# Optimization experiments

Measured on AMD Instinct MI355X. Metric: run time of the kernel, lower is better.

Reference implementation:

```python
import jax, jax.numpy as jnp
import numpy as np

RADIUS_IN = 0.05
RADIUS_OUT = 0.2
NSAMPLE = 32


def setup_inputs() -> dict:
    key = jax.random.key(0)
    k1, k2, k3 = jax.random.split(key, 3)
    B, N, M, C = 2, 16384, 2048, 64
    xyz = jax.random.uniform(k1, (B, N, 3), dtype=jnp.float32)
    new_xyz = jax.random.uniform(k2, (B, M, 3), dtype=jnp.float32)
    features = jax.random.normal(k3, (B, C, N), dtype=jnp.float32)
    return {"xyz": xyz, "new_xyz": new_xyz, "features": features}


def _ball_query_dilated(xyz, new_xyz, r_in, r_out, nsample):
    # xyz: (B,N,3), new_xyz: (B,M,3)
    d2 = jnp.sum((new_xyz[:, :, None, :] - xyz[:, None, :, :]) ** 2, axis=-1)  # (B,M,N)
    mask = (d2 >= r_in * r_in) & (d2 < r_out * r_out)  # dilated shell
    B, M, N = mask.shape
    rank = jnp.cumsum(mask, axis=-1) - 1  # order of each match along N
    cnt = jnp.minimum(jnp.sum(mask, axis=-1), nsample).astype(jnp.int32)  # (B,M)
    # scatter the j-th point index into slot `rank` (overflow slots dumped into pad)
    pos = jnp.where(mask & (rank < nsample), rank, nsample)
    b = jnp.arange(B)[:, None, None]
    m = jnp.arange(M)[None, :, None]
    j = jnp.broadcast_to(jnp.arange(N, dtype=jnp.int32)[None, None, :], (B, M, N))
    idx = jnp.zeros((B, M, nsample + 1), jnp.int32).at[b, m, pos].set(j)[..., :nsample]
    # CUDA kernel fills unused slots with the FIRST matched index (0 if no match)
    slot = jnp.arange(nsample)[None, None, :]
    idx = jnp.where(slot < cnt[..., None], idx, idx[..., :1])
    return cnt, idx


def _group(features, idx):
    # features: (B,C,N), idx: (B,M,S) -> (B,C,M,S)
    B, C, N = features.shape
    _, M, S = idx.shape
    flat = idx.reshape(B, 1, M * S)
    return jnp.take_along_axis(features, flat, axis=2).reshape(B, C, M, S)


def reference(xyz, new_xyz, features):
    idx_cnt, idx = _ball_query_dilated(xyz, new_xyz, RADIUS_IN, RADIUS_OUT, NSAMPLE)
    xyz_t = jnp.transpose(xyz, (0, 2, 1))            # (B,3,N)
    grouped_xyz = _group(xyz_t, idx)                 # (B,3,M,S)
    grouped_xyz = grouped_xyz - jnp.transpose(new_xyz, (0, 2, 1))[..., None]
    grouped_features = _group(features, idx)         # (B,C,M,S)
    new_features = jnp.concatenate([grouped_xyz, grouped_features], axis=1)
    return idx_cnt, new_features
```

## Files before the change

### kernel.cpp

```cpp
#include <hip/hip_runtime.h>
#include <cstdint>

#define BB 2
#define NN 16384
#define MM 2048
#define CC 64
#define SS 32
#define WPB 4

__device__ __forceinline__ float dist2(float qx, float qy, float qz,
                                       float px, float py, float pz) {
    float dx = __fsub_rn(qx, px), dy = __fsub_rn(qy, py), dz = __fsub_rn(qz, pz);
    return __fadd_rn(__fadd_rn(__fmul_rn(dx, dx), __fmul_rn(dy, dy)), __fmul_rn(dz, dz));
}

__global__ __launch_bounds__(256) void prep_fused(
    const float* __restrict__ xyz, const float* __restrict__ f,
    float* __restrict__ ft, float4* __restrict__ xyz4) {
    int bid = blockIdx.x;
    if (bid < 2048) {
        __shared__ float tile[32][33];
        int n0 = (bid & 511) * 32;
        int c0 = ((bid >> 9) & 1) * 32;
        int b = bid >> 10;
        int tx = threadIdx.x & 31, ty = threadIdx.x >> 5;
#pragma unroll
        for (int k = 0; k < 32; k += 8)
            tile[ty + k][tx] = f[((size_t)(b * CC + c0 + ty + k)) * NN + n0 + tx];
        __syncthreads();
#pragma unroll
        for (int k = 0; k < 32; k += 8)
            ft[((size_t)(b * NN + n0 + ty + k)) * CC + c0 + tx] = tile[tx][ty + k];
    } else {
        int i = (bid - 2048) * 256 + threadIdx.x;
        if (i < BB * NN) {
            xyz4[i] = make_float4(xyz[3 * i], xyz[3 * i + 1], xyz[3 * i + 2], 0.f);
        }
    }
}

template <bool FAST>
__global__ __launch_bounds__(64 * WPB) void query_group(
    const float* __restrict__ xyz, const float* __restrict__ new_xyz,
    const float* __restrict__ features, const float* __restrict__ feat_t,
    const float4* __restrict__ xyz4, float* __restrict__ out) {
    constexpr float R_IN2 = 0.05f * 0.05f;
    constexpr float R_OUT2 = 0.2f * 0.2f;
    __shared__ int idxS[WPB][SS];
    __shared__ float fbuf[WPB][SS][CC + 4];

    int lane = threadIdx.x & 63;
    int w = threadIdx.x >> 6;
    int bm = blockIdx.x * WPB + w;
    int b = bm >> 11;
    int m = bm & 2047;

    float qx = new_xyz[(size_t)bm * 3 + 0];
    float qy = new_xyz[(size_t)bm * 3 + 1];
    float qz = new_xyz[(size_t)bm * 3 + 2];

    if (lane == 0) idxS[w][0] = 0;

    unsigned long long below = (1ull << lane) - 1ull;
    int cnt = 0;
    for (int j0 = 0; j0 < NN; j0 += 256) {
        float px[4], py[4], pz[4];
        if (FAST) {
            const float4* base = xyz4 + b * NN + j0 + lane;
#pragma unroll
            for (int u = 0; u < 4; ++u) {
                float4 p = base[u * 64];
                px[u] = p.x; py[u] = p.y; pz[u] = p.z;
            }
        } else {
            const float* pp = xyz + ((size_t)(b * NN + j0 + lane)) * 3;
#pragma unroll
            for (int u = 0; u < 4; ++u) {
                px[u] = pp[u * 192 + 0];
                py[u] = pp[u * 192 + 1];
                pz[u] = pp[u * 192 + 2];
            }
        }
#pragma unroll
        for (int u = 0; u < 4; ++u) {
            float d2 = dist2(qx, qy, qz, px[u], py[u], pz[u]);
            bool inshell = (d2 >= R_IN2) && (d2 < R_OUT2);
            unsigned long long mk = __ballot(inshell);
            if (inshell) {
                int r = cnt + __popcll(mk & below);
                if (r < SS) idxS[w][r] = j0 + u * 64 + lane;
            }
            cnt += __popcll(mk);
        }
        if (cnt >= SS) break;
    }
    if (cnt > SS) cnt = SS;
    if (lane == 0) out[bm] = (float)cnt;

    float* gout = out + BB * MM;

    if (FAST) {
        int s4 = lane >> 4, c4 = lane & 15;
#pragma unroll
        for (int it = 0; it < 8; ++it) {
            int sl = it * 4 + s4;
            int j = (sl < cnt) ? idxS[w][sl] : idxS[w][0];
            const float4* src = (const float4*)(feat_t + ((size_t)b * NN + j) * CC);
            float4 v = src[c4];
            *((float4*)&fbuf[w][sl][c4 * 4]) = v;
        }
    }

    int s = lane & 31, half = lane >> 5;
    int j = (s < cnt) ? idxS[w][s] : idxS[w][0];

    float px, py, pz;
    if (FAST) {
        float4 p = xyz4[b * NN + j];
        px = p.x; py = p.y; pz = p.z;
    } else {
        const float* pp = xyz + ((size_t)(b * NN) + j) * 3;
        px = pp[0]; py = pp[1]; pz = pp[2];
    }

    {
        float v01 = half ? __fsub_rn(py, qy) : __fsub_rn(px, qx);
        gout[((size_t)(b * 67 + half) * MM + m) * SS + s] = v01;
        if (half == 0) {
            gout[((size_t)(b * 67 + 2) * MM + m) * SS + s] = __fsub_rn(pz, qz);
        }
    }

#pragma unroll
    for (int k = 0; k < 32; ++k) {
        int ch = 2 * k + half;
        float v = FAST ? fbuf[w][s][ch]
                       : features[((size_t)(b * CC + ch)) * NN + j];
        gout[((size_t)(b * 67 + 3 + ch) * MM + m) * SS + s] = v;
    }
}

extern "C" void kernel_launch(void* const* d_in, const int* in_sizes, int n_in,
                              void* d_out, int out_size, void* d_ws, size_t ws_size,
                              hipStream_t stream) {
    const float* xyz = (const float*)d_in[0];
    const float* new_xyz = (const float*)d_in[1];
    const float* features = (const float*)d_in[2];
    float* out = (float*)d_out;

    const size_t featT_bytes = (size_t)BB * NN * CC * 4;
    const size_t xyz4_bytes = (size_t)BB * NN * 16;
    bool fast = ws_size >= featT_bytes + xyz4_bytes;

    if (fast) {
        float* feat_t = (float*)d_ws;
        float4* xyz4 = (float4*)((char*)d_ws + featT_bytes);
        prep_fused<<<2048 + 128, 256, 0, stream>>>(xyz, features, feat_t, xyz4);
        query_group<true><<<BB * MM / WPB, 64 * WPB, 0, stream>>>(xyz, new_xyz, features, feat_t, xyz4, out);
    } else {
        query_group<false><<<BB * MM / WPB, 64 * WPB, 0, stream>>>(xyz, new_xyz, features, nullptr, nullptr, out);
    }
}
```

Baseline: 92.23 us.

## Split ball query across eight waves per query with segment merge

Each query point now gets a 512-thread block. Its eight waves each scan one eighth of the N points and record up to 32 shell matches locally. Thread-level prefix logic over the per-wave counts then merges these in order, which shortens the serial scan for queries that find few matches. The grouped-feature write is also reshaped into float4 stores through a shared-memory transpose, and the xyz float4 repacking step is dropped. In exchange, every wave scans its whole segment even when earlier segments already hold 32 matches, so total distance work per query can grow, and the block now uses several barriers.

```diff
diff --git a/kernel.cpp b/kernel.cpp
--- a/kernel.cpp
+++ b/kernel.cpp
@@ -6,7 +6,8 @@
 #define MM 2048
 #define CC 64
 #define SS 32
-#define WPB 4
+#define NWAVE 8
+#define SEG (NN / NWAVE)
 
 __device__ __forceinline__ float dist2(float qx, float qy, float qz,
                                        float px, float py, float pz) {
@@ -14,44 +15,133 @@
     return __fadd_rn(__fadd_rn(__fmul_rn(dx, dx), __fmul_rn(dy, dy)), __fmul_rn(dz, dz));
 }
 
-__global__ __launch_bounds__(256) void prep_fused(
-    const float* __restrict__ xyz, const float* __restrict__ f,
-    float* __restrict__ ft, float4* __restrict__ xyz4) {
+__global__ __launch_bounds__(256) void transpose_feat(
+    const float* __restrict__ f, float* __restrict__ ft) {
+    __shared__ float tile[32][33];
     int bid = blockIdx.x;
-    if (bid < 2048) {
-        __shared__ float tile[32][33];
-        int n0 = (bid & 511) * 32;
-        int c0 = ((bid >> 9) & 1) * 32;
-        int b = bid >> 10;
-        int tx = threadIdx.x & 31, ty = threadIdx.x >> 5;
-#pragma unroll
-        for (int k = 0; k < 32; k += 8)
-            tile[ty + k][tx] = f[((size_t)(b * CC + c0 + ty + k)) * NN + n0 + tx];
-        __syncthreads();
-#pragma unroll
-        for (int k = 0; k < 32; k += 8)
-            ft[((size_t)(b * NN + n0 + ty + k)) * CC + c0 + tx] = tile[tx][ty + k];
-    } else {
-        int i = (bid - 2048) * 256 + threadIdx.x;
-        if (i < BB * NN) {
-            xyz4[i] = make_float4(xyz[3 * i], xyz[3 * i + 1], xyz[3 * i + 2], 0.f);
-        }
-    }
-}
-
-template <bool FAST>
-__global__ __launch_bounds__(64 * WPB) void query_group(
+    int n0 = (bid & 511) * 32;
+    int c0 = ((bid >> 9) & 1) * 32;
+    int b = bid >> 10;
+    int tx = threadIdx.x & 31, ty = threadIdx.x >> 5;
+#pragma unroll
+    for (int k = 0; k < 32; k += 8)
+        tile[ty + k][tx] = f[((size_t)(b * CC + c0 + ty + k)) * NN + n0 + tx];
+    __syncthreads();
+#pragma unroll
+    for (int k = 0; k < 32; k += 8)
+        ft[((size_t)(b * NN + n0 + ty + k)) * CC + c0 + tx] = tile[tx][ty + k];
+}
+
+__global__ __launch_bounds__(512) void qg_kernel(
     const float* __restrict__ xyz, const float* __restrict__ new_xyz,
-    const float* __restrict__ features, const float* __restrict__ feat_t,
-    const float4* __restrict__ xyz4, float* __restrict__ out) {
+    const float* __restrict__ feat_t, float* __restrict__ out) {
     constexpr float R_IN2 = 0.05f * 0.05f;
     constexpr float R_OUT2 = 0.2f * 0.2f;
-    __shared__ int idxS[WPB][SS];
-    __shared__ float fbuf[WPB][SS][CC + 4];
+    __shared__ int idxL[NWAVE][SS];
+    __shared__ int cS[NWAVE];
+    __shared__ int idxS[SS];
+    __shared__ float fbuf[SS][CC + 4];
+
+    int tid = threadIdx.x;
+    int lane = tid & 63;
+    int w = tid >> 6;
+    int bm = blockIdx.x;
+    int b = bm >> 11;
+    int m = bm & 2047;
+
+    float qx = new_xyz[(size_t)bm * 3 + 0];
+    float qy = new_xyz[(size_t)bm * 3 + 1];
+    float qz = new_xyz[(size_t)bm * 3 + 2];
+
+    unsigned long long below = (1ull << lane) - 1ull;
+    int c = 0;
+    int base = w * SEG;
+    for (int j0 = base; j0 < base + SEG; j0 += 256) {
+        float px[4], py[4], pz[4];
+        const float* pp = xyz + ((size_t)(b * NN + j0 + lane)) * 3;
+#pragma unroll
+        for (int u = 0; u < 4; ++u) {
+            px[u] = pp[u * 192 + 0];
+            py[u] = pp[u * 192 + 1];
+            pz[u] = pp[u * 192 + 2];
+        }
+#pragma unroll
+        for (int u = 0; u < 4; ++u) {
+            float d2 = dist2(qx, qy, qz, px[u], py[u], pz[u]);
+            bool inshell = (d2 >= R_IN2) && (d2 < R_OUT2);
+            unsigned long long mk = __ballot(inshell);
+            if (inshell) {
+                int r = c + __popcll(mk & below);
+                if (r < SS) idxL[w][r] = j0 + u * 64 + lane;
+            }
+            c += __popcll(mk);
+        }
+        if (c >= SS) break;
+    }
+    if (c > SS) c = SS;
+    if (lane == 0) cS[w] = c;
+    __syncthreads();
+
+    if (tid < SS) {
+        int r = tid;
+        int acc = 0, pick = -1, off = 0;
+#pragma unroll
+        for (int s = 0; s < NWAVE; ++s) {
+            int cs = cS[s];
+            if (pick < 0 && r < acc + cs) { pick = s; off = r - acc; }
+            acc += cs;
+        }
+        int cnt = acc < SS ? acc : SS;
+        int j;
+        if (r < cnt) {
+            j = idxL[pick][off];
+        } else {
+            int s0 = -1;
+#pragma unroll
+            for (int s = 0; s < NWAVE; ++s)
+                if (s0 < 0 && cS[s] > 0) s0 = s;
+            j = (s0 >= 0) ? idxL[s0][0] : 0;
+        }
+        idxS[r] = j;
+        if (r == 0) out[bm] = (float)cnt;
+    }
+    __syncthreads();
+
+    float* gout = out + BB * MM;
+
+    {
+        int sl = tid >> 4, c4 = tid & 15;
+        float4 v = ((const float4*)(feat_t + ((size_t)b * NN + idxS[sl]) * CC))[c4];
+        *((float4*)&fbuf[sl][c4 * 4]) = v;
+    }
+
+    if (tid < 96) {
+        int ch = tid >> 5, s = tid & 31;
+        int j = idxS[s];
+        float pv = xyz[((size_t)(b * NN) + j) * 3 + ch];
+        float qv = new_xyz[(size_t)bm * 3 + ch];
+        gout[((size_t)(b * 67 + ch) * MM + m) * SS + s] = __fsub_rn(pv, qv);
+    }
+    __syncthreads();
+
+    {
+        int ch = tid >> 3, sg = tid & 7;
+        float4 v = make_float4(fbuf[sg * 4 + 0][ch], fbuf[sg * 4 + 1][ch],
+                               fbuf[sg * 4 + 2][ch], fbuf[sg * 4 + 3][ch]);
+        *((float4*)&gout[((size_t)(b * 67 + 3 + ch) * MM + m) * SS + sg * 4]) = v;
+    }
+}
+
+__global__ __launch_bounds__(256) void query_group_fallback(
+    const float* __restrict__ xyz, const float* __restrict__ new_xyz,
+    const float* __restrict__ features, float* __restrict__ out) {
+    constexpr float R_IN2 = 0.05f * 0.05f;
+    constexpr float R_OUT2 = 0.2f * 0.2f;
+    __shared__ int idxS[4][SS];
 
     int lane = threadIdx.x & 63;
     int w = threadIdx.x >> 6;
-    int bm = blockIdx.x * WPB + w;
+    int bm = blockIdx.x * 4 + w;
     int b = bm >> 11;
     int m = bm & 2047;
 
@@ -65,21 +155,12 @@
     int cnt = 0;
     for (int j0 = 0; j0 < NN; j0 += 256) {
         float px[4], py[4], pz[4];
-        if (FAST) {
-            const float4* base = xyz4 + b * NN + j0 + lane;
-#pragma unroll
-            for (int u = 0; u < 4; ++u) {
-                float4 p = base[u * 64];
-                px[u] = p.x; py[u] = p.y; pz[u] = p.z;
-            }
-        } else {
-            const float* pp = xyz + ((size_t)(b * NN + j0 + lane)) * 3;
-#pragma unroll
-            for (int u = 0; u < 4; ++u) {
-                px[u] = pp[u * 192 + 0];
-                py[u] = pp[u * 192 + 1];
-                pz[u] = pp[u * 192 + 2];
-            }
+        const float* pp = xyz + ((size_t)(b * NN + j0 + lane)) * 3;
+#pragma unroll
+        for (int u = 0; u < 4; ++u) {
+            px[u] = pp[u * 192 + 0];
+            py[u] = pp[u * 192 + 1];
+            pz[u] = pp[u * 192 + 2];
         }
 #pragma unroll
         for (int u = 0; u < 4; ++u) {
@@ -98,44 +179,17 @@
     if (lane == 0) out[bm] = (float)cnt;
 
     float* gout = out + BB * MM;
-
-    if (FAST) {
-        int s4 = lane >> 4, c4 = lane & 15;
-#pragma unroll
-        for (int it = 0; it < 8; ++it) {
-            int sl = it * 4 + s4;
-            int j = (sl < cnt) ? idxS[w][sl] : idxS[w][0];
-            const float4* src = (const float4*)(feat_t + ((size_t)b * NN + j) * CC);
-            float4 v = src[c4];
-            *((float4*)&fbuf[w][sl][c4 * 4]) = v;
-        }
-    }
-
     int s = lane & 31, half = lane >> 5;
     int j = (s < cnt) ? idxS[w][s] : idxS[w][0];
-
-    float px, py, pz;
-    if (FAST) {
-        float4 p = xyz4[b * NN + j];
-        px = p.x; py = p.y; pz = p.z;
-    } else {
-        const float* pp = xyz + ((size_t)(b * NN) + j) * 3;
-        px = pp[0]; py = pp[1]; pz = pp[2];
-    }
-
-    {
-        float v01 = half ? __fsub_rn(py, qy) : __fsub_rn(px, qx);
-        gout[((size_t)(b * 67 + half) * MM + m) * SS + s] = v01;
-        if (half == 0) {
-            gout[((size_t)(b * 67 + 2) * MM + m) * SS + s] = __fsub_rn(pz, qz);
-        }
-    }
-
+    const float* pp = xyz + ((size_t)(b * NN) + j) * 3;
+    float px = pp[0], py = pp[1], pz = pp[2];
+    float v01 = half ? __fsub_rn(py, qy) : __fsub_rn(px, qx);
+    gout[((size_t)(b * 67 + half) * MM + m) * SS + s] = v01;
+    if (half == 0) gout[((size_t)(b * 67 + 2) * MM + m) * SS + s] = __fsub_rn(pz, qz);
 #pragma unroll
     for (int k = 0; k < 32; ++k) {
         int ch = 2 * k + half;
-        float v = FAST ? fbuf[w][s][ch]
-                       : features[((size_t)(b * CC + ch)) * NN + j];
+        float v = features[((size_t)(b * CC + ch)) * NN + j];
         gout[((size_t)(b * 67 + 3 + ch) * MM + m) * SS + s] = v;
     }
 }
@@ -149,15 +203,13 @@
     float* out = (float*)d_out;
 
     const size_t featT_bytes = (size_t)BB * NN * CC * 4;
-    const size_t xyz4_bytes = (size_t)BB * NN * 16;
-    bool fast = ws_size >= featT_bytes + xyz4_bytes;
+    bool fast = ws_size >= featT_bytes;
 
     if (fast) {
         float* feat_t = (float*)d_ws;
-        float4* xyz4 = (float4*)((char*)d_ws + featT_bytes);
-        prep_fused<<<2048 + 128, 256, 0, stream>>>(xyz, features, feat_t, xyz4);
-        query_group<true><<<BB * MM / WPB, 64 * WPB, 0, stream>>>(xyz, new_xyz, features, feat_t, xyz4, out);
+        transpose_feat<<<2048, 256, 0, stream>>>(features, feat_t);
+        qg_kernel<<<BB * MM, 512, 0, stream>>>(xyz, new_xyz, feat_t, out);
     } else {
-        query_group<false><<<BB * MM / WPB, 64 * WPB, 0, stream>>>(xyz, new_xyz, features, nullptr, nullptr, out);
-    }
-}
+        query_group_fallback<<<BB * MM / 4, 256, 0, stream>>>(xyz, new_xyz, features, out);
+    }
+}
```

Result: slower. 104.2 us (+13.0%).
